# Optimization experiments

Hardware: AMD Instinct MI355X
Metric: run time of the kernel (lower is better)

## Reference

```python
import jax, jax.numpy as jnp
import numpy as np

B, S, DIM, NUM_TYPES = 2048, 50, 128, 32000
EPS = 1e-5


def _l2norm(x):
    # torch F.normalize(p=2, dim=-1, eps=1e-5): x / max(||x||_2, eps)
    n = jnp.sqrt(jnp.sum(x * x, axis=-1, keepdims=True))
    return x / jnp.maximum(n, EPS)


def setup_inputs() -> dict:
    key = jax.random.key(0)
    ks = jax.random.split(key, 8)
    enc_output = jax.random.normal(ks[0], (B, S, DIM), dtype=jnp.float32)
    event_type = jax.random.randint(ks[1], (B, S), 0, NUM_TYPES, dtype=jnp.int64)
    user_type = jax.random.randint(ks[2], (B,), 0, NUM_TYPES, dtype=jnp.int64)
    # xavier_normal_ for [num_types, dim] weight: std = sqrt(2/(fan_in+fan_out))
    std = float(np.sqrt(2.0 / (DIM + NUM_TYPES)))
    W1 = jax.random.normal(ks[3], (NUM_TYPES, DIM), dtype=jnp.float32) * std
    W2 = jax.random.normal(ks[4], (NUM_TYPES, DIM), dtype=jnp.float32) * std
    W3 = jax.random.normal(ks[5], (NUM_TYPES, DIM), dtype=jnp.float32) * std
    W4 = jax.random.normal(ks[6], (NUM_TYPES, DIM), dtype=jnp.float32) * std
    one = jnp.ones((1,), dtype=jnp.float32)
    return {"enc_output": enc_output, "event_type": event_type, "user_type": user_type,
            "W1": W1, "W2": W2, "W3": W3, "W4": W4,
            "a": one, "b": one, "c": one, "d": one}


def reference(enc_output, event_type, user_type, W1, W2, W3, W4, a, b, c, d):
    # mean over time axis
    data = jnp.mean(enc_output, axis=1)  # [B, dim]
    p1 = _l2norm(jnp.einsum("bd,td->bt", data, W1))  # [B, num_types]
    p2 = _l2norm(jnp.einsum("bd,td->bt", data, W2))
    p3 = _l2norm(jnp.einsum("bd,td->bt", data, W3))
    p4 = _l2norm(jnp.einsum("bd,td->bt", data, W4))
    out = jnp.tanh(p1 * a + p2 * b + p3 * c + p4 * d)

    # Vectorized replacement of the per-sample python loop:
    # target_[i][e-1] = 0 for all nonzero events e; pad column absorbs zeros.
    bsz, num_types = out.shape[0], W1.shape[0]
    idx = jnp.where(event_type > 0, event_type - 1, num_types)  # [B, S]
    rows = jnp.arange(bsz)[:, None]
    target = jnp.ones((bsz, num_types + 1), dtype=out.dtype)
    target = target.at[rows, idx].set(0.0)
    target = target[:, :num_types]
    return out, target
```

## Files before the change

### kernel.cpp

```cpp
#include <hip/hip_runtime.h>
#include <stdint.h>

#define B_SZ 2048
#define S_SZ 50
#define D_SZ 128
#define T_SZ 32000
#define K4D 512

typedef __attribute__((ext_vector_type(8))) short short8v;
typedef __attribute__((ext_vector_type(4))) float floatx4;

__device__ __forceinline__ unsigned short f2bf(float f) {
  uint32_t u = __float_as_uint(f);
  uint32_t r = (u + 0x7fffu + ((u >> 16) & 1u)) >> 16;
  return (unsigned short)r;
}

__global__ __launch_bounds__(256) void k_mean(const float* __restrict__ enc,
                                              float* __restrict__ data) {
  int wid = threadIdx.x >> 6;
  int lane = threadIdx.x & 63;
  int b = blockIdx.x * 4 + wid;
  const float* src = enc + (size_t)b * (S_SZ * D_SZ) + lane * 2;
  float s0 = 0.f, s1 = 0.f;
#pragma unroll
  for (int s = 0; s < S_SZ; ++s) {
    float2 v = *(const float2*)(src + s * D_SZ);
    s0 += v.x; s1 += v.y;
  }
  float2 o; o.x = s0 * (1.f / 50.f); o.y = s1 * (1.f / 50.f);
  *(float2*)(data + (size_t)b * D_SZ + lane * 2) = o;
}

__global__ __launch_bounds__(256) void k_cast(const float* __restrict__ W1, const float* __restrict__ W2,
                                              const float* __restrict__ W3, const float* __restrict__ W4,
                                              unsigned short* __restrict__ w4) {
  int c = blockIdx.x * 256 + threadIdx.x;
  int e = c * 8;
  int t = e >> 9;
  int col = e & 511;
  int i = col >> 7;
  int d = col & 127;
  const float* src = (i == 0) ? W1 : (i == 1) ? W2 : (i == 2) ? W3 : W4;
  src += (size_t)t * 128 + d;
  float4 a = *(const float4*)src;
  float4 b = *(const float4*)(src + 4);
  union { short8v v; unsigned short u[8]; } pk;
  pk.u[0] = f2bf(a.x); pk.u[1] = f2bf(a.y); pk.u[2] = f2bf(a.z); pk.u[3] = f2bf(a.w);
  pk.u[4] = f2bf(b.x); pk.u[5] = f2bf(b.y); pk.u[6] = f2bf(b.z); pk.u[7] = f2bf(b.w);
  *(short8v*)(w4 + (size_t)t * 512 + col) = pk.v;
}

__global__ __launch_bounds__(256) void k_gram(const unsigned short* __restrict__ w4,
                                              float* __restrict__ G) {
  __shared__ unsigned short WT[128 * 72];
  int tid = threadIdx.x;
  int lane = tid & 63, wid = tid >> 6;
  int mat = blockIdx.x / 50;
  int chunk = blockIdx.x % 50;
  int t0 = chunk * 640;

  floatx4 acc[2][8];
#pragma unroll
  for (int aa = 0; aa < 2; ++aa)
#pragma unroll
    for (int n = 0; n < 8; ++n) acc[aa][n] = (floatx4){0.f, 0.f, 0.f, 0.f};

  for (int ks = 0; ks < 10; ++ks) {
    __syncthreads();
    const unsigned short* srow = w4 + (size_t)(t0 + ks * 64 + lane) * 512 + mat * 128;
#pragma unroll
    for (int r = 0; r < 4; ++r) {
      int ch = wid + r * 4;
      uint4 v = *(const uint4*)(srow + ch * 8);
      int dbase = ch * 8;
      WT[(dbase + 0) * 72 + lane] = (unsigned short)(v.x & 0xffff);
      WT[(dbase + 1) * 72 + lane] = (unsigned short)(v.x >> 16);
      WT[(dbase + 2) * 72 + lane] = (unsigned short)(v.y & 0xffff);
      WT[(dbase + 3) * 72 + lane] = (unsigned short)(v.y >> 16);
      WT[(dbase + 4) * 72 + lane] = (unsigned short)(v.z & 0xffff);
      WT[(dbase + 5) * 72 + lane] = (unsigned short)(v.z >> 16);
      WT[(dbase + 6) * 72 + lane] = (unsigned short)(v.w & 0xffff);
      WT[(dbase + 7) * 72 + lane] = (unsigned short)(v.w >> 16);
    }
    __syncthreads();
#pragma unroll
    for (int kk = 0; kk < 2; ++kk) {
      int kb = kk * 32 + (lane >> 4) * 8;
      short8v af[2], bfr[8];
#pragma unroll
      for (int aa = 0; aa < 2; ++aa) {
        int row = (wid * 2 + aa) * 16 + (lane & 15);
        af[aa] = *(const short8v*)&WT[row * 72 + kb];
      }
#pragma unroll
      for (int n = 0; n < 8; ++n) {
        int row = n * 16 + (lane & 15);
        bfr[n] = *(const short8v*)&WT[row * 72 + kb];
      }
#pragma unroll
      for (int aa = 0; aa < 2; ++aa)
#pragma unroll
        for (int n = 0; n < 8; ++n)
          acc[aa][n] = __builtin_amdgcn_mfma_f32_16x16x32_bf16(af[aa], bfr[n], acc[aa][n], 0, 0, 0);
    }
  }
  int g8 = lane >> 4, lc = lane & 15;
#pragma unroll
  for (int aa = 0; aa < 2; ++aa)
#pragma unroll
    for (int n = 0; n < 8; ++n)
#pragma unroll
      for (int q = 0; q < 4; ++q) {
        int row = (wid * 2 + aa) * 16 + g8 * 4 + q;
        int col = n * 16 + lc;
        unsafeAtomicAdd(&G[mat * 16384 + row * 128 + col], acc[aa][n][q]);
      }
}

__global__ __launch_bounds__(256) void k_norm(const float* __restrict__ data, const float* __restrict__ G,
                                              const float* __restrict__ pa, const float* __restrict__ pb,
                                              const float* __restrict__ pc, const float* __restrict__ pd,
                                              unsigned short* __restrict__ data4) {
  __shared__ float dsh[16][132];
  __shared__ float Gch[32][132];
  __shared__ float sc[16][4];
  int tid = threadIdx.x;
  int b0 = blockIdx.x * 16;

  {
    int e = tid * 8;
    int rr = e >> 7, cc = e & 127;
    float4 v0 = *(const float4*)(data + (size_t)(b0 + rr) * 128 + cc);
    float4 v1 = *(const float4*)(data + (size_t)(b0 + rr) * 128 + cc + 4);
    *(float4*)&dsh[rr][cc] = v0;
    *(float4*)&dsh[rr][cc + 4] = v1;
  }
  int bl = tid >> 4, sub = tid & 15;
  float ss[4];
#pragma unroll
  for (int i = 0; i < 4; ++i) ss[i] = 0.f;

#pragma unroll
  for (int i = 0; i < 4; ++i) {
    for (int jc = 0; jc < 4; ++jc) {
      __syncthreads();
      {
        int e = tid * 16;
        int rr = e >> 7, cc = e & 127;
        const float* gsrc = G + i * 16384 + (jc * 32 + rr) * 128 + cc;
#pragma unroll
        for (int q = 0; q < 4; ++q)
          *(float4*)&Gch[rr][cc + q * 4] = *(const float4*)(gsrc + q * 4);
      }
      __syncthreads();
#pragma unroll
      for (int j2 = 0; j2 < 2; ++j2) {
        int jl = sub + j2 * 16;
        float tmp = 0.f;
#pragma unroll 8
        for (int k4 = 0; k4 < 32; ++k4) {
          float4 g = *(const float4*)&Gch[jl][k4 * 4];
          float4 dd = *(const float4*)&dsh[bl][k4 * 4];
          tmp += g.x * dd.x + g.y * dd.y + g.z * dd.z + g.w * dd.w;
        }
        ss[i] += dsh[bl][jc * 32 + jl] * tmp;
      }
    }
  }
#pragma unroll
  for (int i = 0; i < 4; ++i) {
    ss[i] += __shfl_xor(ss[i], 1);
    ss[i] += __shfl_xor(ss[i], 2);
    ss[i] += __shfl_xor(ss[i], 4);
    ss[i] += __shfl_xor(ss[i], 8);
  }
  if (sub == 0) {
    float cf0 = pa[0], cf1 = pb[0], cf2 = pc[0], cf3 = pd[0];
    sc[bl][0] = cf0 / fmaxf(sqrtf(ss[0]), 1e-5f);
    sc[bl][1] = cf1 / fmaxf(sqrtf(ss[1]), 1e-5f);
    sc[bl][2] = cf2 / fmaxf(sqrtf(ss[2]), 1e-5f);
    sc[bl][3] = cf3 / fmaxf(sqrtf(ss[3]), 1e-5f);
  }
  __syncthreads();
  for (int e = tid; e < 16 * 512; e += 256) {
    int r = e >> 9, col = e & 511;
    int i = col >> 7, d = col & 127;
    float v = dsh[r][d] * sc[r][i];
    data4[(size_t)(b0 + r) * 512 + col] = f2bf(v);
  }
}

__global__ __launch_bounds__(256, 2) void k_gemm(const unsigned short* __restrict__ data4,
                                                 const unsigned short* __restrict__ w4,
                                                 float* __restrict__ out, float* __restrict__ target) {
  __shared__ unsigned short As[128 * 64];
  __shared__ unsigned short Bs[128 * 64];
  int tid = threadIdx.x, lane = tid & 63, wid = tid >> 6;
  int bid = blockIdx.x;
  int sb = (bid & 7) * 500 + (bid >> 3);
  int tn = sb / 16, tm = sb % 16;
  int m0 = tm * 128, n0 = tn * 128;
  int srow = lane >> 3, slot = lane & 7;
  int wrr = (wid >> 1) * 64, wcc = (wid & 1) * 64;

  floatx4 acc[4][4];
#pragma unroll
  for (int m = 0; m < 4; ++m)
#pragma unroll
    for (int n = 0; n < 4; ++n) acc[m][n] = (floatx4){0.f, 0.f, 0.f, 0.f};

  const char* Abase = (const char*)data4;
  const char* Bbase = (const char*)w4;

  for (int kt = 0; kt < 8; ++kt) {
    if (kt) __syncthreads();
#pragma unroll
    for (int u = 0; u < 4; ++u) {
      int row = wid * 32 + u * 8 + srow;
      int sw = ((slot ^ (row & 7)) * 16);
      const char* ga = Abase + (size_t)(m0 + row) * 1024 + kt * 128 + sw;
      const char* gb = Bbase + (size_t)(n0 + row) * 1024 + kt * 128 + sw;
      int lbo = __builtin_amdgcn_readfirstlane(wid * 4096 + u * 1024);
      __builtin_amdgcn_global_load_lds((const __attribute__((address_space(1))) void*)ga,
                                       (__attribute__((address_space(3))) void*)((char*)As + lbo), 16, 0, 0);
      __builtin_amdgcn_global_load_lds((const __attribute__((address_space(1))) void*)gb,
                                       (__attribute__((address_space(3))) void*)((char*)Bs + lbo), 16, 0, 0);
    }
    __syncthreads();
    int g8 = lane >> 4;
#pragma unroll
    for (int kk = 0; kk < 2; ++kk) {
      short8v af[4], bfr[4];
#pragma unroll
      for (int m = 0; m < 4; ++m) {
        int r = wrr + m * 16 + (lane & 15);
        int byteoff = r * 128 + (((kk * 4 + g8) ^ (r & 7)) * 16);
        af[m] = *(const short8v*)((const char*)As + byteoff);
      }
#pragma unroll
      for (int n = 0; n < 4; ++n) {
        int r = wcc + n * 16 + (lane & 15);
        int byteoff = r * 128 + (((kk * 4 + g8) ^ (r & 7)) * 16);
        bfr[n] = *(const short8v*)((const char*)Bs + byteoff);
      }
#pragma unroll
      for (int m = 0; m < 4; ++m)
#pragma unroll
        for (int n = 0; n < 4; ++n)
          acc[m][n] = __builtin_amdgcn_mfma_f32_16x16x32_bf16(af[m], bfr[n], acc[m][n], 0, 0, 0);
    }
  }
  int g8 = lane >> 4, lc = lane & 15;
#pragma unroll
  for (int m = 0; m < 4; ++m)
#pragma unroll
    for (int n = 0; n < 4; ++n)
#pragma unroll
      for (int q = 0; q < 4; ++q) {
        int row = m0 + wrr + m * 16 + g8 * 4 + q;
        int col = n0 + wcc + n * 16 + lc;
        float x = acc[m][n][q];
        float e2 = __expf(2.f * x);
        size_t idx = (size_t)row * 32000 + col;
        out[idx] = (e2 - 1.f) / (e2 + 1.f);
        target[idx] = 1.0f;
      }
}

__global__ __launch_bounds__(256) void k_scatter(const int* __restrict__ ev, float* __restrict__ target) {
  int g = blockIdx.x * 256 + threadIdx.x;
  if (g >= B_SZ * S_SZ) return;
  int b = g / 50;
  int et = ev[g];
  if (et > 0) target[(size_t)b * 32000 + (et - 1)] = 0.f;
}

extern "C" void kernel_launch(void* const* d_in, const int* in_sizes, int n_in,
                              void* d_out, int out_size, void* d_ws, size_t ws_size,
                              hipStream_t stream) {
  const float* enc = (const float*)d_in[0];
  const int* ev = (const int*)d_in[1];
  const float* W1 = (const float*)d_in[3];
  const float* W2 = (const float*)d_in[4];
  const float* W3 = (const float*)d_in[5];
  const float* W4 = (const float*)d_in[6];
  const float* pa = (const float*)d_in[7];
  const float* pb = (const float*)d_in[8];
  const float* pc = (const float*)d_in[9];
  const float* pd = (const float*)d_in[10];

  float* out = (float*)d_out;
  float* target = out + (size_t)B_SZ * T_SZ;

  char* ws = (char*)d_ws;
  float* data = (float*)ws;
  unsigned short* data4 = (unsigned short*)(ws + (1 << 20));
  float* G = (float*)(ws + 3 * (1 << 20));
  unsigned short* w4 = (unsigned short*)(ws + 4 * (1 << 20));

  hipMemsetAsync(G, 0, 4 * 128 * 128 * sizeof(float), stream);
  k_mean<<<512, 256, 0, stream>>>(enc, data);
  k_cast<<<8000, 256, 0, stream>>>(W1, W2, W3, W4, w4);
  k_gram<<<200, 256, 0, stream>>>(w4, G);
  k_norm<<<128, 256, 0, stream>>>(data, G, pa, pb, pc, pd, data4);
  k_gemm<<<4000, 256, 0, stream>>>(data4, w4, out, target);
  k_scatter<<<400, 256, 0, stream>>>(ev, target);
}
```

Before: 807.2 us.

## Replace gram atomics with partial-sum reduction and move target fill out of GEMM

The Gram kernel now writes per-block partial 128x128 results to a workspace buffer, and a new reduction kernel sums the 50 chunks per matrix. This removes the float atomics and the memset. The target ones-fill is taken out of the GEMM epilogue and merged with the event scatter into one row-per-block fill kernel, which shrinks the GEMM's store traffic. GEMM launch bounds are raised to 3 blocks per SM to allow more occupancy, at the cost of tighter register limits and one extra kernel launch.

```diff
diff --git a/kernel.cpp b/kernel.cpp
--- a/kernel.cpp
+++ b/kernel.cpp
@@ -5,7 +5,6 @@
 #define S_SZ 50
 #define D_SZ 128
 #define T_SZ 32000
-#define K4D 512
 
 typedef __attribute__((ext_vector_type(8))) short short8v;
 typedef __attribute__((ext_vector_type(4))) float floatx4;
@@ -52,7 +51,7 @@
 }
 
 __global__ __launch_bounds__(256) void k_gram(const unsigned short* __restrict__ w4,
-                                              float* __restrict__ G) {
+                                              float* __restrict__ Gp) {
   __shared__ unsigned short WT[128 * 72];
   int tid = threadIdx.x;
   int lane = tid & 63, wid = tid >> 6;
@@ -105,6 +104,7 @@
           acc[aa][n] = __builtin_amdgcn_mfma_f32_16x16x32_bf16(af[aa], bfr[n], acc[aa][n], 0, 0, 0);
     }
   }
+  float* gp = Gp + (size_t)blockIdx.x * 16384;
   int g8 = lane >> 4, lc = lane & 15;
 #pragma unroll
   for (int aa = 0; aa < 2; ++aa)
@@ -114,8 +114,22 @@
       for (int q = 0; q < 4; ++q) {
         int row = (wid * 2 + aa) * 16 + g8 * 4 + q;
         int col = n * 16 + lc;
-        unsafeAtomicAdd(&G[mat * 16384 + row * 128 + col], acc[aa][n][q]);
-      }
+        gp[row * 128 + col] = acc[aa][n][q];
+      }
+}
+
+__global__ __launch_bounds__(256) void k_greduce(const float* __restrict__ Gp,
+                                                 float* __restrict__ G) {
+  int mat = blockIdx.x >> 4;
+  int e = ((blockIdx.x & 15) * 256 + threadIdx.x) * 4;
+  const float* src = Gp + (size_t)(mat * 50) * 16384 + e;
+  float4 s = {0.f, 0.f, 0.f, 0.f};
+#pragma unroll 10
+  for (int c = 0; c < 50; ++c) {
+    float4 v = *(const float4*)(src + (size_t)c * 16384);
+    s.x += v.x; s.y += v.y; s.z += v.z; s.w += v.w;
+  }
+  *(float4*)(G + (size_t)mat * 16384 + e) = s;
 }
 
 __global__ __launch_bounds__(256) void k_norm(const float* __restrict__ data, const float* __restrict__ G,
@@ -191,9 +205,9 @@
   }
 }
 
-__global__ __launch_bounds__(256, 2) void k_gemm(const unsigned short* __restrict__ data4,
+__global__ __launch_bounds__(256, 3) void k_gemm(const unsigned short* __restrict__ data4,
                                                  const unsigned short* __restrict__ w4,
-                                                 float* __restrict__ out, float* __restrict__ target) {
+                                                 float* __restrict__ out) {
   __shared__ unsigned short As[128 * 64];
   __shared__ unsigned short Bs[128 * 64];
   int tid = threadIdx.x, lane = tid & 63, wid = tid >> 6;
@@ -262,18 +276,22 @@
         int col = n0 + wcc + n * 16 + lc;
         float x = acc[m][n][q];
         float e2 = __expf(2.f * x);
-        size_t idx = (size_t)row * 32000 + col;
-        out[idx] = (e2 - 1.f) / (e2 + 1.f);
-        target[idx] = 1.0f;
-      }
-}
-
-__global__ __launch_bounds__(256) void k_scatter(const int* __restrict__ ev, float* __restrict__ target) {
-  int g = blockIdx.x * 256 + threadIdx.x;
-  if (g >= B_SZ * S_SZ) return;
-  int b = g / 50;
-  int et = ev[g];
-  if (et > 0) target[(size_t)b * 32000 + (et - 1)] = 0.f;
+        out[(size_t)row * 32000 + col] = (e2 - 1.f) / (e2 + 1.f);
+      }
+}
+
+__global__ __launch_bounds__(256) void k_fill(const int* __restrict__ ev,
+                                              float* __restrict__ target) {
+  int b = blockIdx.x;
+  float4* row4 = (float4*)(target + (size_t)b * 32000);
+  float4 one = {1.f, 1.f, 1.f, 1.f};
+#pragma unroll 4
+  for (int j = threadIdx.x; j < 8000; j += 256) row4[j] = one;
+  __syncthreads();
+  if (threadIdx.x < 50) {
+    int et = ev[b * 50 + threadIdx.x];
+    if (et > 0) ((float*)row4)[et - 1] = 0.f;
+  }
 }
 
 extern "C" void kernel_launch(void* const* d_in, const int* in_sizes, int n_in,
@@ -298,12 +316,13 @@
   unsigned short* data4 = (unsigned short*)(ws + (1 << 20));
   float* G = (float*)(ws + 3 * (1 << 20));
   unsigned short* w4 = (unsigned short*)(ws + 4 * (1 << 20));
-
-  hipMemsetAsync(G, 0, 4 * 128 * 128 * sizeof(float), stream);
+  float* Gp = (float*)(ws + 36 * (size_t)(1 << 20));
+
   k_mean<<<512, 256, 0, stream>>>(enc, data);
   k_cast<<<8000, 256, 0, stream>>>(W1, W2, W3, W4, w4);
-  k_gram<<<200, 256, 0, stream>>>(w4, G);
+  k_gram<<<200, 256, 0, stream>>>(w4, Gp);
+  k_greduce<<<64, 256, 0, stream>>>(Gp, G);
   k_norm<<<128, 256, 0, stream>>>(data, G, pa, pb, pc, pd, data4);
-  k_gemm<<<4000, 256, 0, stream>>>(data4, w4, out, target);
-  k_scatter<<<400, 256, 0, stream>>>(ev, target);
-}
+  k_gemm<<<4000, 256, 0, stream>>>(data4, w4, out);
+  k_fill<<<2048, 256, 0, stream>>>(ev, target);
+}
```

Measured after the change: 738.4 us. -8.5%, faster.
